# Performance work log

Hardware: AMD Instinct MI355X
Metric: run time of the kernel (lower is better)

Reference implementation:

```python
import jax, jax.numpy as jnp
import numpy as np

B, S, D = 2, 2048, 1024
H, KS, VS = 16, 64, 64

def setup_inputs() -> dict:
    key = jax.random.key(0)
    ks = jax.random.split(key, 11)
    s = 1.0 / np.sqrt(D)
    return {
        "query": jax.random.normal(ks[0], (B, S, D), jnp.float32),
        "key":   jax.random.normal(ks[1], (B, S, D), jnp.float32),
        "value": jax.random.normal(ks[2], (B, S, D), jnp.float32),
        # weights stored [in, out] (transpose of torch Linear)
        "Wq": jax.random.normal(ks[3], (D, H * KS), jnp.float32) * s,
        "bq": jnp.zeros((H * KS,), jnp.float32),
        "Wk": jax.random.normal(ks[4], (D, H * KS), jnp.float32) * s,
        "bk": jnp.zeros((H * KS,), jnp.float32),
        "Wv": jax.random.normal(ks[5], (D, H * VS), jnp.float32) * s,
        "bv": jnp.zeros((H * VS,), jnp.float32),
        "Wo": jax.random.normal(ks[6], (H * VS, D), jnp.float32) * s,
        "bo": jnp.zeros((D,), jnp.float32),
    }

def reference(query, key, value, Wq, bq, Wk, bk, Wv, bv, Wo, bo):
    b = query.shape[0]
    # projections + split heads -> [B, H, S, d]
    Q = (query @ Wq + bq).reshape(b, -1, H, KS).transpose(0, 2, 1, 3)
    K = (key   @ Wk + bk).reshape(b, -1, H, KS).transpose(0, 2, 1, 3)
    V = (value @ Wv + bv).reshape(b, -1, H, VS).transpose(0, 2, 1, 3)
    scores = jnp.einsum('bhqd,bhkd->bhqk', Q, K) / jnp.sqrt(jnp.float32(KS))
    attn = jax.nn.softmax(scores, axis=-1)  # dropout_rate=0.0 -> identity
    ctx = jnp.einsum('bhqk,bhkd->bhqd', attn, V)  # [B,H,S,VS]
    ctx = ctx.transpose(0, 2, 1, 3).reshape(b, attn.shape[-1], H * VS)
    out = ctx @ Wo + bo
    return out, attn
```

## Files before the change

### kernel.cpp

```cpp
#include <hip/hip_runtime.h>
#include <stdint.h>


typedef _Float16 f16;
typedef f16 f16x4 __attribute__((ext_vector_type(4)));
typedef f16 f16x8 __attribute__((ext_vector_type(8)));
typedef float f32x4 __attribute__((ext_vector_type(4)));
typedef uint32_t u32;
typedef u32 u32x4 __attribute__((ext_vector_type(4)));

#define L2E 1.4426950408889634f

__device__ __forceinline__ void gload16(const void* g, void* l) {
    __builtin_amdgcn_global_load_lds((__attribute__((address_space(1))) void*)g,
                                     (__attribute__((address_space(3))) void*)l,
                                     16, 0, 0);
}

__global__ __launch_bounds__(256) void k_cvt(const float* __restrict__ q,
                                             const float* __restrict__ k,
                                             const float* __restrict__ v,
                                             f16* __restrict__ dst)
{
    int z = blockIdx.z;
    const float* s = (z == 0) ? q : (z == 1) ? k : v;
    size_t i = (size_t)blockIdx.x * 256 + threadIdx.x;
    float4 f = ((const float4*)s)[i];
    f16x4 o = {(f16)f.x, (f16)f.y, (f16)f.z, (f16)f.w};
    *(f16x4*)(dst + (size_t)z * 4194304 + i * 4) = o;
}

__global__ __launch_bounds__(256) void k_wtrans(const float* __restrict__ w0,
                                                const float* __restrict__ w1,
                                                const float* __restrict__ w2,
                                                const float* __restrict__ w3,
                                                f16* __restrict__ wt)
{
    __shared__ f16 t[64][72];
    int z = blockIdx.z;
    const float* W = (z == 0) ? w0 : (z == 1) ? w1 : (z == 2) ? w2 : w3;
    f16* outp = wt + (size_t)z * 1048576;
    int tx = blockIdx.x, ty = blockIdx.y, tid = threadIdx.x;
#pragma unroll
    for (int r4 = 0; r4 < 4; r4++) {
        int row = r4 * 16 + (tid >> 4);
        int col = (tid & 15) * 4;
        float4 f = *(const float4*)(W + (size_t)(ty * 64 + row) * 1024 + tx * 64 + col);
        t[col + 0][row] = (f16)f.x; t[col + 1][row] = (f16)f.y;
        t[col + 2][row] = (f16)f.z; t[col + 3][row] = (f16)f.w;
    }
    __syncthreads();
#pragma unroll
    for (int cc = 0; cc < 2; cc++) {
        int c = tid + cc * 256;
        int row = c >> 3, ch = c & 7;
        f16x8 vv;
#pragma unroll
        for (int j = 0; j < 8; j++) vv[j] = t[row][ch * 8 + j];
        *(f16x8*)(outp + (size_t)(tx * 64 + row) * 1024 + ty * 64 + ch * 8) = vv;
    }
}

__global__ __launch_bounds__(256) void k_gemm(const f16* __restrict__ Ab,
                                              const f16* __restrict__ Wtb,
                                              const float* __restrict__ b0,
                                              const float* __restrict__ b1,
                                              const float* __restrict__ b2,
                                              void* __restrict__ o0,
                                              void* __restrict__ o1,
                                              int proj)
{
    __shared__ __align__(16) char As[16384];
    __shared__ __align__(16) char Bs[16384];
    const int tid = threadIdx.x;
    const int wv = tid >> 6, ln = tid & 63, lg = ln >> 4, li = ln & 15;
    const int m0 = blockIdx.y * 128, n0 = blockIdx.x * 128;
    const int wm = (wv >> 1) * 64, wn = (wv & 1) * 64;

    const f16* A; const f16* Bt; const float* bias; int mode;
    if (proj) {
        int z = blockIdx.z;
        A = Ab + (size_t)z * 4194304;
        Bt = Wtb + (size_t)z * 1048576;
        bias = (z == 0) ? b0 : (z == 1) ? b1 : b2;
        mode = (z == 2) ? 1 : 0;
    } else { A = Ab; Bt = Wtb; bias = b0; mode = 2; }

    const char* gA[4]; const char* gB[4];
#pragma unroll
    for (int c = 0; c < 4; c++) {
        int r = (wv * 4 + c) * 8 + (ln >> 3);
        int j = (ln & 7) ^ (r & 7);
        gA[c] = (const char*)A  + (size_t)(m0 + r) * 2048 + j * 16;
        gB[c] = (const char*)Bt + (size_t)(n0 + r) * 2048 + j * 16;
    }

    f32x4 acc[4][4] = {};
    for (int kt = 0; kt < 16; kt++) {
        __syncthreads();
#pragma unroll
        for (int c = 0; c < 4; c++) {
            gload16(gA[c] + kt * 128, As + (wv * 4 + c) * 1024);
            gload16(gB[c] + kt * 128, Bs + (wv * 4 + c) * 1024);
        }
        __syncthreads();
#pragma unroll
        for (int kk = 0; kk < 2; kk++) {
            f16x8 af[4], bf[4];
#pragma unroll
            for (int mi = 0; mi < 4; mi++) {
                int row = wm + mi * 16 + li;
                af[mi] = *(const f16x8*)(As + row * 128 + (((kk * 4 + lg) ^ (row & 7)) * 16));
            }
#pragma unroll
            for (int ni = 0; ni < 4; ni++) {
                int row = wn + ni * 16 + li;
                bf[ni] = *(const f16x8*)(Bs + row * 128 + (((kk * 4 + lg) ^ (row & 7)) * 16));
            }
#pragma unroll
            for (int mi = 0; mi < 4; mi++)
#pragma unroll
                for (int ni = 0; ni < 4; ni++)
                    acc[mi][ni] = __builtin_amdgcn_mfma_f32_16x16x32_f16(af[mi], bf[ni], acc[mi][ni], 0, 0, 0);
        }
    }

    float bvs[4];
#pragma unroll
    for (int ni = 0; ni < 4; ni++) bvs[ni] = bias[n0 + wn + ni * 16 + li];

    if (mode == 2) {
        float* O = (float*)o0;
#pragma unroll
        for (int mi = 0; mi < 4; mi++)
#pragma unroll
            for (int ni = 0; ni < 4; ni++) {
                int n = n0 + wn + ni * 16 + li;
#pragma unroll
                for (int r = 0; r < 4; r++) {
                    int m = m0 + wm + mi * 16 + lg * 4 + r;
                    O[(size_t)m * 1024 + n] = acc[mi][ni][r] + bvs[ni];
                }
            }
    } else if (mode == 0) {
        f16* O = (f16*)o0 + (size_t)blockIdx.z * 4194304;
#pragma unroll
        for (int mi = 0; mi < 4; mi++)
#pragma unroll
            for (int ni = 0; ni < 4; ni++) {
                int n = n0 + wn + ni * 16 + li;
                int h = n >> 6, d = n & 63;
#pragma unroll
                for (int r = 0; r < 4; r++) {
                    int m = m0 + wm + mi * 16 + lg * 4 + r;
                    int b = m >> 11, s = m & 2047;
                    O[(((size_t)b * 16 + h) * 2048 + s) * 64 + d] = (f16)(acc[mi][ni][r] + bvs[ni]);
                }
            }
    } else {
        f16* O = (f16*)o1;
#pragma unroll
        for (int mi = 0; mi < 4; mi++)
#pragma unroll
            for (int ni = 0; ni < 4; ni++) {
                int n = n0 + wn + ni * 16 + li;
                int h = n >> 6, d = n & 63;
                int mb = m0 + wm + mi * 16 + lg * 4;
                int b = mb >> 11, s = mb & 2047;
                f16x4 pk;
#pragma unroll
                for (int r = 0; r < 4; r++) pk[r] = (f16)(acc[mi][ni][r] + bvs[ni]);
                *(f16x4*)(O + (((size_t)b * 16 + h) * 64 + d) * 2048 + s) = pk;
            }
    }
}

__global__ __launch_bounds__(256, 3) void k_attn(const f16* __restrict__ Qb,
                                                 const f16* __restrict__ Kb,
                                                 const f16* __restrict__ Vt,
                                                 float* __restrict__ attn,
                                                 f16* __restrict__ ctx)
{
    __shared__ __align__(16) char Ks[16384];
    __shared__ __align__(16) char Ps[4][2048];
    const int tid = threadIdx.x, wv = tid >> 6, ln = tid & 63, lg = ln >> 4, li = ln & 15;
    const int bid = blockIdx.x;
    const int kk = bid >> 3;
    const int bh = (bid & 7) * 4 + (kk >> 5);
    const int q0 = (kk & 31) * 64 + wv * 16;

    const char* KbB = (const char*)Kb + (size_t)bh * 262144;
    const char* VtB = (const char*)Vt + (size_t)bh * 262144;

    const f16* qrow = Qb + ((size_t)bh * 2048 + q0 + li) * 64 + lg * 8;
    f16x8 aq0 = *(const f16x8*)(qrow);
    f16x8 aq1 = *(const f16x8*)(qrow + 32);
#pragma unroll
    for (int j = 0; j < 8; j++) {
        aq0[j] = (f16)((float)aq0[j] * 0.125f);
        aq1[j] = (f16)((float)aq1[j] * 0.125f);
    }

    float lacc[4] = {0.f, 0.f, 0.f, 0.f};
    {
        int swp[4];
        const char* gp[4];
#pragma unroll
        for (int t = 0; t < 4; t++) {
            int c = tid + t * 256;
            int r = c >> 3, j = c & 7;
            swp[t] = r * 128 + ((j ^ (r & 7)) * 16);
            gp[t] = KbB + (size_t)r * 128 + j * 16;
        }
        u32x4 s[4];
#pragma unroll
        for (int t = 0; t < 4; t++) s[t] = *(const u32x4*)(gp[t]);
        for (int kt = 0; kt < 16; kt++) {
            __syncthreads();
#pragma unroll
            for (int t = 0; t < 4; t++) *(u32x4*)(Ks + swp[t]) = s[t];
            __syncthreads();
            if (kt + 1 < 16) {
#pragma unroll
                for (int t = 0; t < 4; t++) s[t] = *(const u32x4*)(gp[t] + (size_t)(kt + 1) * 16384);
            }
#pragma unroll
            for (int cf = 0; cf < 8; cf++) {
                int row = cf * 16 + li;
                f16x8 ak0 = *(const f16x8*)(Ks + row * 128 + ((lg ^ (row & 7)) * 16));
                f16x8 ak1 = *(const f16x8*)(Ks + row * 128 + (((4 + lg) ^ (row & 7)) * 16));
                f32x4 z = {0.f, 0.f, 0.f, 0.f};
                z = __builtin_amdgcn_mfma_f32_16x16x32_f16(ak0, aq0, z, 0, 0, 0);
                z = __builtin_amdgcn_mfma_f32_16x16x32_f16(ak1, aq1, z, 0, 0, 0);
                lacc[cf & 3] += exp2f(z[0] * L2E) + exp2f(z[1] * L2E)
                              + exp2f(z[2] * L2E) + exp2f(z[3] * L2E);
            }
        }
    }
    float l_ = (lacc[0] + lacc[1]) + (lacc[2] + lacc[3]);
    l_ += __shfl_xor(l_, 16);
    l_ += __shfl_xor(l_, 32);
    const float inv_l = 1.0f / l_;
    float* aBase = attn + ((size_t)bh * 2048 + q0) * 2048;
    char* Pw = Ps[wv];

    const int srowb = ln >> 4;
    const int skv = (ln & 15) * 4;
    const int sldso = ((((ln & 15) >> 1)) * 16) + (ln & 1) * 8;

    f32x4 cacc[4] = {};
    const int r0 = tid >> 3, j0 = tid & 7;
    const int r1 = (tid + 256) >> 3, j1 = (tid + 256) & 7;
    const int sw0 = r0 * 128 + ((j0 ^ (r0 & 7)) * 16);
    const int sw1 = r1 * 128 + ((j1 ^ (r1 & 7)) * 16);
    u32x4 sk0 = *(const u32x4*)(KbB + (size_t)r0 * 128 + j0 * 16);
    u32x4 sk1 = *(const u32x4*)(KbB + (size_t)r1 * 128 + j1 * 16);
    for (int kt = 0; kt < 32; kt++) {
        __syncthreads();
        *(u32x4*)(Ks + sw0) = sk0;
        *(u32x4*)(Ks + sw1) = sk1;
        __syncthreads();
        if (kt + 1 < 32) {
            sk0 = *(const u32x4*)(KbB + (size_t)((kt + 1) * 64 + r0) * 128 + j0 * 16);
            sk1 = *(const u32x4*)(KbB + (size_t)((kt + 1) * 64 + r1) * 128 + j1 * 16);
        }
        f16x8 vf[4][2];
#pragma unroll
        for (int df = 0; df < 4; df++) {
            const char* vr = VtB + (size_t)(df * 16 + li) * 4096 + kt * 128 + lg * 16;
            vf[df][0] = *(const f16x8*)vr;
            vf[df][1] = *(const f16x8*)(vr + 64);
        }
        f32x4 zz[4];
#pragma unroll
        for (int cf = 0; cf < 4; cf++) {
            int row = cf * 16 + li;
            f16x8 ak0 = *(const f16x8*)(Ks + row * 128 + ((lg ^ (row & 7)) * 16));
            f16x8 ak1 = *(const f16x8*)(Ks + row * 128 + (((4 + lg) ^ (row & 7)) * 16));
            f32x4 z = {0.f, 0.f, 0.f, 0.f};
            z = __builtin_amdgcn_mfma_f32_16x16x32_f16(ak0, aq0, z, 0, 0, 0);
            z = __builtin_amdgcn_mfma_f32_16x16x32_f16(ak1, aq1, z, 0, 0, 0);
            zz[cf] = z;
        }
#pragma unroll
        for (int cf = 0; cf < 4; cf++) {
            float p0 = exp2f(zz[cf][0] * L2E) * inv_l;
            float p1 = exp2f(zz[cf][1] * L2E) * inv_l;
            float p2 = exp2f(zz[cf][2] * L2E) * inv_l;
            float p3 = exp2f(zz[cf][3] * L2E) * inv_l;
            f16x4 pk = {(f16)p0, (f16)p1, (f16)p2, (f16)p3};
            int c = cf * 2 + (lg >> 1);
            *(f16x4*)(Pw + li * 128 + ((c ^ (li & 7)) * 16) + (lg & 1) * 8) = pk;
        }
#pragma unroll
        for (int j = 0; j < 4; j++) {
            int row = j * 4 + srowb;
            f16x4 pv4 = *(const f16x4*)(Pw + row * 128 + ((sldso) ^ ((row & 7) * 16)));
            f32x4 fv = {(float)pv4[0], (float)pv4[1], (float)pv4[2], (float)pv4[3]};
            __builtin_nontemporal_store(fv, (f32x4*)(aBase + (size_t)row * 2048 + kt * 64 + skv));
        }
#pragma unroll
        for (int s2 = 0; s2 < 2; s2++) {
            f16x8 bp = *(const f16x8*)(Pw + li * 128 + (((s2 * 4 + lg) ^ (li & 7)) * 16));
#pragma unroll
            for (int df = 0; df < 4; df++)
                cacc[df] = __builtin_amdgcn_mfma_f32_16x16x32_f16(vf[df][s2], bp, cacc[df], 0, 0, 0);
        }
    }

    const int b = bh >> 4, h = bh & 15;
#pragma unroll
    for (int df = 0; df < 4; df++) {
        f16x4 pk;
#pragma unroll
        for (int r = 0; r < 4; r++) pk[r] = (f16)cacc[df][r];
        size_t mrow = (size_t)b * 2048 + q0 + li;
        size_t n = (size_t)h * 64 + df * 16 + lg * 4;
        *(f16x4*)(ctx + mrow * 1024 + n) = pk;
    }
}

extern "C" void kernel_launch(void* const* d_in, const int* in_sizes, int n_in,
                              void* d_out, int out_size, void* d_ws, size_t ws_size,
                              hipStream_t stream)
{
    const float* q  = (const float*)d_in[0];
    const float* k  = (const float*)d_in[1];
    const float* v  = (const float*)d_in[2];
    const float* Wq = (const float*)d_in[3];
    const float* bq = (const float*)d_in[4];
    const float* Wk = (const float*)d_in[5];
    const float* bk = (const float*)d_in[6];
    const float* Wv = (const float*)d_in[7];
    const float* bv = (const float*)d_in[8];
    const float* Wo = (const float*)d_in[9];
    const float* bo = (const float*)d_in[10];

    f16* W = (f16*)d_ws;
    float* out = (float*)d_out;
    float* attn = out + 4194304;

    f16* X   = W;
    f16* Wt  = W + 12582912;
    f16* QKb = W + 16777216;
    f16* Vt  = W + 25165824;
    f16* ctx = W + 29360128;

    k_cvt<<<dim3(4096, 1, 3), 256, 0, stream>>>(q, k, v, X);
    k_wtrans<<<dim3(16, 16, 4), 256, 0, stream>>>(Wq, Wk, Wv, Wo, Wt);
    k_gemm<<<dim3(8, 32, 3), 256, 0, stream>>>(X, Wt, bq, bk, bv, QKb, Vt, 1);
    k_attn<<<dim3(1024), 256, 0, stream>>>(QKb, QKb + 4194304, Vt, attn, ctx);
    k_gemm<<<dim3(8, 32, 1), 256, 0, stream>>>(ctx, Wt + 3145728, bo, bo, bo, out, nullptr, 0);
}
```

Baseline: 257.9 us.

## Process two query tiles per attention block, fusing B's row-sum into A's pass

Each attention block now handles two 64-query groups. The softmax denominator for the second group is accumulated during the first group's main pass, reusing the same K tiles in LDS. This removes one separate K-only statistics pass per pair of tiles and halves the grid to 512 blocks with a 2-block occupancy hint. The trade-off is fewer blocks in flight and higher register pressure from the extra Q fragments and accumulators.

```diff
diff --git a/kernel.cpp b/kernel.cpp
--- a/kernel.cpp
+++ b/kernel.cpp
@@ -175,7 +175,7 @@
     }
 }
 
-__global__ __launch_bounds__(256, 3) void k_attn(const f16* __restrict__ Qb,
+__global__ __launch_bounds__(256, 2) void k_attn(const f16* __restrict__ Qb,
                                                  const f16* __restrict__ Kb,
                                                  const f16* __restrict__ Vt,
                                                  float* __restrict__ attn,
@@ -186,19 +186,28 @@
     const int tid = threadIdx.x, wv = tid >> 6, ln = tid & 63, lg = ln >> 4, li = ln & 15;
     const int bid = blockIdx.x;
     const int kk = bid >> 3;
-    const int bh = (bid & 7) * 4 + (kk >> 5);
-    const int q0 = (kk & 31) * 64 + wv * 16;
+    const int bh = (bid & 7) * 4 + (kk >> 4);
+    const int q0A = (kk & 15) * 128 + wv * 16;
+    const int q0B = q0A + 64;
 
     const char* KbB = (const char*)Kb + (size_t)bh * 262144;
     const char* VtB = (const char*)Vt + (size_t)bh * 262144;
 
-    const f16* qrow = Qb + ((size_t)bh * 2048 + q0 + li) * 64 + lg * 8;
-    f16x8 aq0 = *(const f16x8*)(qrow);
-    f16x8 aq1 = *(const f16x8*)(qrow + 32);
-#pragma unroll
-    for (int j = 0; j < 8; j++) {
-        aq0[j] = (f16)((float)aq0[j] * 0.125f);
-        aq1[j] = (f16)((float)aq1[j] * 0.125f);
+    f16x8 aqA0, aqA1, aqB0, aqB1;
+    {
+        const f16* qra = Qb + ((size_t)bh * 2048 + q0A + li) * 64 + lg * 8;
+        aqA0 = *(const f16x8*)(qra);
+        aqA1 = *(const f16x8*)(qra + 32);
+        const f16* qrb = Qb + ((size_t)bh * 2048 + q0B + li) * 64 + lg * 8;
+        aqB0 = *(const f16x8*)(qrb);
+        aqB1 = *(const f16x8*)(qrb + 32);
+#pragma unroll
+        for (int j = 0; j < 8; j++) {
+            aqA0[j] = (f16)((float)aqA0[j] * 0.125f);
+            aqA1[j] = (f16)((float)aqA1[j] * 0.125f);
+            aqB0[j] = (f16)((float)aqB0[j] * 0.125f);
+            aqB1[j] = (f16)((float)aqB1[j] * 0.125f);
+        }
     }
 
     float lacc[4] = {0.f, 0.f, 0.f, 0.f};
@@ -230,83 +239,98 @@
                 f16x8 ak0 = *(const f16x8*)(Ks + row * 128 + ((lg ^ (row & 7)) * 16));
                 f16x8 ak1 = *(const f16x8*)(Ks + row * 128 + (((4 + lg) ^ (row & 7)) * 16));
                 f32x4 z = {0.f, 0.f, 0.f, 0.f};
-                z = __builtin_amdgcn_mfma_f32_16x16x32_f16(ak0, aq0, z, 0, 0, 0);
-                z = __builtin_amdgcn_mfma_f32_16x16x32_f16(ak1, aq1, z, 0, 0, 0);
+                z = __builtin_amdgcn_mfma_f32_16x16x32_f16(ak0, aqA0, z, 0, 0, 0);
+                z = __builtin_amdgcn_mfma_f32_16x16x32_f16(ak1, aqA1, z, 0, 0, 0);
                 lacc[cf & 3] += exp2f(z[0] * L2E) + exp2f(z[1] * L2E)
                               + exp2f(z[2] * L2E) + exp2f(z[3] * L2E);
             }
         }
     }
-    float l_ = (lacc[0] + lacc[1]) + (lacc[2] + lacc[3]);
-    l_ += __shfl_xor(l_, 16);
-    l_ += __shfl_xor(l_, 32);
-    const float inv_l = 1.0f / l_;
-    float* aBase = attn + ((size_t)bh * 2048 + q0) * 2048;
+    float lA = (lacc[0] + lacc[1]) + (lacc[2] + lacc[3]);
+    lA += __shfl_xor(lA, 16);
+    lA += __shfl_xor(lA, 32);
+    const float inv_lA = 1.0f / lA;
+
+    float* aBaseA = attn + ((size_t)bh * 2048 + q0A) * 2048;
+    float* aBaseB = attn + ((size_t)bh * 2048 + q0B) * 2048;
     char* Pw = Ps[wv];
 
     const int srowb = ln >> 4;
     const int skv = (ln & 15) * 4;
-    const int sldso = ((((ln & 15) >> 1)) * 16) + (ln & 1) * 8;
-
-    f32x4 cacc[4] = {};
+    const int sldso = (((ln & 15) >> 1) * 16) + (ln & 1) * 8;
+
     const int r0 = tid >> 3, j0 = tid & 7;
     const int r1 = (tid + 256) >> 3, j1 = (tid + 256) & 7;
     const int sw0 = r0 * 128 + ((j0 ^ (r0 & 7)) * 16);
     const int sw1 = r1 * 128 + ((j1 ^ (r1 & 7)) * 16);
-    u32x4 sk0 = *(const u32x4*)(KbB + (size_t)r0 * 128 + j0 * 16);
-    u32x4 sk1 = *(const u32x4*)(KbB + (size_t)r1 * 128 + j1 * 16);
-    for (int kt = 0; kt < 32; kt++) {
-        __syncthreads();
-        *(u32x4*)(Ks + sw0) = sk0;
-        *(u32x4*)(Ks + sw1) = sk1;
-        __syncthreads();
-        if (kt + 1 < 32) {
-            sk0 = *(const u32x4*)(KbB + (size_t)((kt + 1) * 64 + r0) * 128 + j0 * 16);
-            sk1 = *(const u32x4*)(KbB + (size_t)((kt + 1) * 64 + r1) * 128 + j1 * 16);
-        }
-        f16x8 vf[4][2];
-#pragma unroll
-        for (int df = 0; df < 4; df++) {
-            const char* vr = VtB + (size_t)(df * 16 + li) * 4096 + kt * 128 + lg * 16;
-            vf[df][0] = *(const f16x8*)vr;
-            vf[df][1] = *(const f16x8*)(vr + 64);
-        }
-        f32x4 zz[4];
-#pragma unroll
-        for (int cf = 0; cf < 4; cf++) {
-            int row = cf * 16 + li;
-            f16x8 ak0 = *(const f16x8*)(Ks + row * 128 + ((lg ^ (row & 7)) * 16));
-            f16x8 ak1 = *(const f16x8*)(Ks + row * 128 + (((4 + lg) ^ (row & 7)) * 16));
-            f32x4 z = {0.f, 0.f, 0.f, 0.f};
-            z = __builtin_amdgcn_mfma_f32_16x16x32_f16(ak0, aq0, z, 0, 0, 0);
-            z = __builtin_amdgcn_mfma_f32_16x16x32_f16(ak1, aq1, z, 0, 0, 0);
-            zz[cf] = z;
-        }
-#pragma unroll
-        for (int cf = 0; cf < 4; cf++) {
-            float p0 = exp2f(zz[cf][0] * L2E) * inv_l;
-            float p1 = exp2f(zz[cf][1] * L2E) * inv_l;
-            float p2 = exp2f(zz[cf][2] * L2E) * inv_l;
-            float p3 = exp2f(zz[cf][3] * L2E) * inv_l;
-            f16x4 pk = {(f16)p0, (f16)p1, (f16)p2, (f16)p3};
-            int c = cf * 2 + (lg >> 1);
-            *(f16x4*)(Pw + li * 128 + ((c ^ (li & 7)) * 16) + (lg & 1) * 8) = pk;
-        }
-#pragma unroll
-        for (int j = 0; j < 4; j++) {
-            int row = j * 4 + srowb;
-            f16x4 pv4 = *(const f16x4*)(Pw + row * 128 + ((sldso) ^ ((row & 7) * 16)));
-            f32x4 fv = {(float)pv4[0], (float)pv4[1], (float)pv4[2], (float)pv4[3]};
-            __builtin_nontemporal_store(fv, (f32x4*)(aBase + (size_t)row * 2048 + kt * 64 + skv));
-        }
-#pragma unroll
-        for (int s2 = 0; s2 < 2; s2++) {
-            f16x8 bp = *(const f16x8*)(Pw + li * 128 + (((s2 * 4 + lg) ^ (li & 7)) * 16));
-#pragma unroll
-            for (int df = 0; df < 4; df++)
-                cacc[df] = __builtin_amdgcn_mfma_f32_16x16x32_f16(vf[df][s2], bp, cacc[df], 0, 0, 0);
-        }
-    }
+
+    f32x4 cacc[4] = {};
+    lacc[0] = lacc[1] = lacc[2] = lacc[3] = 0.f;
+    {
+        u32x4 sk0 = *(const u32x4*)(KbB + (size_t)r0 * 128 + j0 * 16);
+        u32x4 sk1 = *(const u32x4*)(KbB + (size_t)r1 * 128 + j1 * 16);
+        for (int kt = 0; kt < 32; kt++) {
+            __syncthreads();
+            *(u32x4*)(Ks + sw0) = sk0;
+            *(u32x4*)(Ks + sw1) = sk1;
+            __syncthreads();
+            if (kt + 1 < 32) {
+                sk0 = *(const u32x4*)(KbB + (size_t)((kt + 1) * 64 + r0) * 128 + j0 * 16);
+                sk1 = *(const u32x4*)(KbB + (size_t)((kt + 1) * 64 + r1) * 128 + j1 * 16);
+            }
+            f16x8 vf[4][2];
+#pragma unroll
+            for (int df = 0; df < 4; df++) {
+                const char* vr = VtB + (size_t)(df * 16 + li) * 4096 + kt * 128 + lg * 16;
+                vf[df][0] = *(const f16x8*)vr;
+                vf[df][1] = *(const f16x8*)(vr + 64);
+            }
+            f32x4 zzA[4];
+#pragma unroll
+            for (int cf = 0; cf < 4; cf++) {
+                int row = cf * 16 + li;
+                f16x8 ak0 = *(const f16x8*)(Ks + row * 128 + ((lg ^ (row & 7)) * 16));
+                f16x8 ak1 = *(const f16x8*)(Ks + row * 128 + (((4 + lg) ^ (row & 7)) * 16));
+                f32x4 zA = {0.f, 0.f, 0.f, 0.f};
+                zA = __builtin_amdgcn_mfma_f32_16x16x32_f16(ak0, aqA0, zA, 0, 0, 0);
+                zA = __builtin_amdgcn_mfma_f32_16x16x32_f16(ak1, aqA1, zA, 0, 0, 0);
+                zzA[cf] = zA;
+                f32x4 zB = {0.f, 0.f, 0.f, 0.f};
+                zB = __builtin_amdgcn_mfma_f32_16x16x32_f16(ak0, aqB0, zB, 0, 0, 0);
+                zB = __builtin_amdgcn_mfma_f32_16x16x32_f16(ak1, aqB1, zB, 0, 0, 0);
+                lacc[cf] += exp2f(zB[0] * L2E) + exp2f(zB[1] * L2E)
+                          + exp2f(zB[2] * L2E) + exp2f(zB[3] * L2E);
+            }
+#pragma unroll
+            for (int cf = 0; cf < 4; cf++) {
+                float p0 = exp2f(zzA[cf][0] * L2E) * inv_lA;
+                float p1 = exp2f(zzA[cf][1] * L2E) * inv_lA;
+                float p2 = exp2f(zzA[cf][2] * L2E) * inv_lA;
+                float p3 = exp2f(zzA[cf][3] * L2E) * inv_lA;
+                f16x4 pk = {(f16)p0, (f16)p1, (f16)p2, (f16)p3};
+                int c = cf * 2 + (lg >> 1);
+                *(f16x4*)(Pw + li * 128 + ((c ^ (li & 7)) * 16) + (lg & 1) * 8) = pk;
+            }
+#pragma unroll
+            for (int j = 0; j < 4; j++) {
+                int row = j * 4 + srowb;
+                f16x4 pv4 = *(const f16x4*)(Pw + row * 128 + (sldso ^ ((row & 7) * 16)));
+                f32x4 fv = {(float)pv4[0], (float)pv4[1], (float)pv4[2], (float)pv4[3]};
+                __builtin_nontemporal_store(fv, (f32x4*)(aBaseA + (size_t)row * 2048 + kt * 64 + skv));
+            }
+#pragma unroll
+            for (int s2 = 0; s2 < 2; s2++) {
+                f16x8 bp = *(const f16x8*)(Pw + li * 128 + (((s2 * 4 + lg) ^ (li & 7)) * 16));
+#pragma unroll
+                for (int df = 0; df < 4; df++)
+                    cacc[df] = __builtin_amdgcn_mfma_f32_16x16x32_f16(vf[df][s2], bp, cacc[df], 0, 0, 0);
+            }
+        }
+    }
+    float lB = (lacc[0] + lacc[1]) + (lacc[2] + lacc[3]);
+    lB += __shfl_xor(lB, 16);
+    lB += __shfl_xor(lB, 32);
+    const float inv_lB = 1.0f / lB;
 
     const int b = bh >> 4, h = bh & 15;
 #pragma unroll
@@ -314,7 +338,75 @@
         f16x4 pk;
 #pragma unroll
         for (int r = 0; r < 4; r++) pk[r] = (f16)cacc[df][r];
-        size_t mrow = (size_t)b * 2048 + q0 + li;
+        size_t mrow = (size_t)b * 2048 + q0A + li;
+        size_t n = (size_t)h * 64 + df * 16 + lg * 4;
+        *(f16x4*)(ctx + mrow * 1024 + n) = pk;
+    }
+
+#pragma unroll
+    for (int df = 0; df < 4; df++) cacc[df] = (f32x4){0.f, 0.f, 0.f, 0.f};
+    {
+        u32x4 sk0 = *(const u32x4*)(KbB + (size_t)r0 * 128 + j0 * 16);
+        u32x4 sk1 = *(const u32x4*)(KbB + (size_t)r1 * 128 + j1 * 16);
+        for (int kt = 0; kt < 32; kt++) {
+            __syncthreads();
+            *(u32x4*)(Ks + sw0) = sk0;
+            *(u32x4*)(Ks + sw1) = sk1;
+            __syncthreads();
+            if (kt + 1 < 32) {
+                sk0 = *(const u32x4*)(KbB + (size_t)((kt + 1) * 64 + r0) * 128 + j0 * 16);
+                sk1 = *(const u32x4*)(KbB + (size_t)((kt + 1) * 64 + r1) * 128 + j1 * 16);
+            }
+            f16x8 vf[4][2];
+#pragma unroll
+            for (int df = 0; df < 4; df++) {
+                const char* vr = VtB + (size_t)(df * 16 + li) * 4096 + kt * 128 + lg * 16;
+                vf[df][0] = *(const f16x8*)vr;
+                vf[df][1] = *(const f16x8*)(vr + 64);
+            }
+            f32x4 zz[4];
+#pragma unroll
+            for (int cf = 0; cf < 4; cf++) {
+                int row = cf * 16 + li;
+                f16x8 ak0 = *(const f16x8*)(Ks + row * 128 + ((lg ^ (row & 7)) * 16));
+                f16x8 ak1 = *(const f16x8*)(Ks + row * 128 + (((4 + lg) ^ (row & 7)) * 16));
+                f32x4 z = {0.f, 0.f, 0.f, 0.f};
+                z = __builtin_amdgcn_mfma_f32_16x16x32_f16(ak0, aqB0, z, 0, 0, 0);
+                z = __builtin_amdgcn_mfma_f32_16x16x32_f16(ak1, aqB1, z, 0, 0, 0);
+                zz[cf] = z;
+            }
+#pragma unroll
+            for (int cf = 0; cf < 4; cf++) {
+                float p0 = exp2f(zz[cf][0] * L2E) * inv_lB;
+                float p1 = exp2f(zz[cf][1] * L2E) * inv_lB;
+                float p2 = exp2f(zz[cf][2] * L2E) * inv_lB;
+                float p3 = exp2f(zz[cf][3] * L2E) * inv_lB;
+                f16x4 pk = {(f16)p0, (f16)p1, (f16)p2, (f16)p3};
+                int c = cf * 2 + (lg >> 1);
+                *(f16x4*)(Pw + li * 128 + ((c ^ (li & 7)) * 16) + (lg & 1) * 8) = pk;
+            }
+#pragma unroll
+            for (int j = 0; j < 4; j++) {
+                int row = j * 4 + srowb;
+                f16x4 pv4 = *(const f16x4*)(Pw + row * 128 + (sldso ^ ((row & 7) * 16)));
+                f32x4 fv = {(float)pv4[0], (float)pv4[1], (float)pv4[2], (float)pv4[3]};
+                __builtin_nontemporal_store(fv, (f32x4*)(aBaseB + (size_t)row * 2048 + kt * 64 + skv));
+            }
+#pragma unroll
+            for (int s2 = 0; s2 < 2; s2++) {
+                f16x8 bp = *(const f16x8*)(Pw + li * 128 + (((s2 * 4 + lg) ^ (li & 7)) * 16));
+#pragma unroll
+                for (int df = 0; df < 4; df++)
+                    cacc[df] = __builtin_amdgcn_mfma_f32_16x16x32_f16(vf[df][s2], bp, cacc[df], 0, 0, 0);
+            }
+        }
+    }
+#pragma unroll
+    for (int df = 0; df < 4; df++) {
+        f16x4 pk;
+#pragma unroll
+        for (int r = 0; r < 4; r++) pk[r] = (f16)cacc[df][r];
+        size_t mrow = (size_t)b * 2048 + q0B + li;
         size_t n = (size_t)h * 64 + df * 16 + lg * 4;
         *(f16x4*)(ctx + mrow * 1024 + n) = pk;
     }
@@ -349,6 +441,6 @@
     k_cvt<<<dim3(4096, 1, 3), 256, 0, stream>>>(q, k, v, X);
     k_wtrans<<<dim3(16, 16, 4), 256, 0, stream>>>(Wq, Wk, Wv, Wo, Wt);
     k_gemm<<<dim3(8, 32, 3), 256, 0, stream>>>(X, Wt, bq, bk, bv, QKb, Vt, 1);
-    k_attn<<<dim3(1024), 256, 0, stream>>>(QKb, QKb + 4194304, Vt, attn, ctx);
+    k_attn<<<dim3(512), 256, 0, stream>>>(QKb, QKb + 4194304, Vt, attn, ctx);
     k_gemm<<<dim3(8, 32, 1), 256, 0, stream>>>(ctx, Wt + 3145728, bo, bo, bo, out, nullptr, 0);
 }
```

Measured after the change: 263.5 us. +2.2%, slower.
